# Performance work log

Hardware: AMD Instinct MI355X
Metric: run time of the kernel (lower is better)

The kernel has to match this reference:

```python
import jax, jax.numpy as jnp
import numpy as np

EPS = 1e-5


def _rln(x, w, b, m1w, m1b, m2w, m2b):
    # Revised LayerNorm (DehazeFormer): per-sample stats over (C,H,W)
    mean = jnp.mean(x, axis=(1, 2, 3), keepdims=True)            # [b,1,1,1]
    std = jnp.sqrt(jnp.mean((x - mean) ** 2, axis=(1, 2, 3), keepdims=True) + EPS)
    normed = (x - mean) / std * w + b                            # [b,C,H,W]
    rescale = std * m1w + m1b                                    # 1x1 conv from 1 channel
    rebias = mean * m2w + m2b
    return normed, rescale, rebias


def _pconv(x, W, b):
    # 1x1 conv as channel contraction: W [out,in], x [b,in,h,w]
    return jnp.einsum('oi,bihw->bohw', W, x) + b[None, :, None, None]


def setup_inputs() -> dict:
    key = jax.random.key(0)
    ks = jax.random.split(key, 24)
    B, C, H, W = 8, 96, 128, 128
    p = lambda k, shp, s=0.02: (jax.random.normal(k, shp, dtype=jnp.float32) * s)
    inp = {
        'x_u': jax.random.normal(ks[0], (B, C, H, W), dtype=jnp.float32),
        'x_d': jax.random.normal(ks[1], (B, C, H, W), dtype=jnp.float32),
        # RLN (u)
        'nw_u': jnp.ones((1, C, 1, 1), jnp.float32),
        'nb_u': jnp.zeros((1, C, 1, 1), jnp.float32),
        'm1w_u': p(ks[2], (1, C, 1, 1)), 'm1b_u': p(ks[3], (1, C, 1, 1)),
        'm2w_u': p(ks[4], (1, C, 1, 1)), 'm2b_u': p(ks[5], (1, C, 1, 1)),
        # RLN (d)
        'nw_d': jnp.ones((1, C, 1, 1), jnp.float32),
        'nb_d': jnp.zeros((1, C, 1, 1), jnp.float32),
        'm1w_d': p(ks[6], (1, C, 1, 1)), 'm1b_d': p(ks[7], (1, C, 1, 1)),
        'm2w_d': p(ks[8], (1, C, 1, 1)), 'm2b_d': p(ks[9], (1, C, 1, 1)),
        # 1x1 qkv convs
        'Wqkv_u': p(ks[10], (2 * C, C)), 'bqkv_u': jnp.zeros((2 * C,), jnp.float32),
        'Wqkv_d': p(ks[11], (2 * C, C)), 'bqkv_d': jnp.zeros((2 * C,), jnp.float32),
        # learned scalar scales
        'scale_h': jnp.ones((1,), jnp.float32),
        'scale_w': jnp.ones((1,), jnp.float32),
        'scale_c': jnp.ones((1,), jnp.float32),
    }
    return inp


def reference(x_u, x_d,
              nw_u, nb_u, m1w_u, m1b_u, m2w_u, m2b_u,
              nw_d, nb_d, m1w_d, m1b_d, m2w_d, m2b_d,
              Wqkv_u, bqkv_u, Wqkv_d, bqkv_d,
              scale_h, scale_w, scale_c):
    x_d_norm, resc_d, bias_d = _rln(x_d, nw_d, nb_d, m1w_d, m1b_d, m2w_d, m2b_d)
    x_u_norm, resc_u, bias_u = _rln(x_u, nw_u, nb_u, m1w_u, m1b_u, m2w_u, m2b_u)

    q_u, v_u = jnp.split(_pconv(x_u_norm, Wqkv_u, bqkv_u), 2, axis=1)
    k_d, v_d = jnp.split(_pconv(x_d_norm, Wqkv_d, bqkv_d), 2, axis=1)

    q_h, q_w, q_c = jnp.split(q_u, 3, axis=1)
    k_h, k_w, k_c = jnp.split(k_d, 3, axis=1)
    vu_h, vu_w, vu_c = jnp.split(v_u, 3, axis=1)
    vd_h, vd_w, vd_c = jnp.split(v_d, 3, axis=1)

    # ---- height-axis attention: per (b,w), scores over h x h ----
    A_h = jax.nn.softmax(jnp.einsum('bciw,bcjw->bwij', q_h, k_h) * scale_h[0], axis=-1)
    d2u_h = jnp.einsum('bwij,bcjw->bciw', A_h, vd_h)            # attn @ v_d
    u2d_h = jnp.einsum('bwij,bciw->bcjw', A_h, vu_h)            # attn^T @ v_u

    # ---- width-axis attention: per (b,h), scores over w x w ----
    S_w = jnp.einsum('bchi,bchj->bhij', q_w, k_w) * scale_w[0]
    d2u_w = jnp.einsum('bhij,bchj->bchi', jax.nn.softmax(S_w, axis=-1), vd_w)
    # softmax(S_w^T, -1) @ v_u  ==  softmax over axis -2, contracted over i
    u2d_w = jnp.einsum('bhij,bchi->bchj', jax.nn.softmax(S_w, axis=-2), vu_w)

    # ---- channel-axis attention: per b, scores over c x c ----
    b, c, h, w = q_c.shape
    qc = q_c.reshape(b, c, h * w)
    kc = k_c.reshape(b, c, h * w)
    A_c = jax.nn.softmax(jnp.einsum('bcn,bdn->bcd', qc, kc) * scale_c[0], axis=-1)
    d2u_c = jnp.einsum('bcd,bdn->bcn', A_c, vd_c.reshape(b, c, h * w)).reshape(b, c, h, w)
    # NOTE: original code uses the same (non-transposed) softmax for u2d_c
    u2d_c = jnp.einsum('bcd,bdn->bcn', A_c, vu_c.reshape(b, c, h * w)).reshape(b, c, h, w)

    x_d2u = jnp.concatenate([d2u_h, d2u_w, d2u_c], axis=1)
    x_u2d = jnp.concatenate([u2d_h, u2d_w, u2d_c], axis=1)

    out_u = x_d2u * resc_u + bias_u + x_u
    out_d = x_u2d * resc_d + bias_d + x_d
    return out_u + out_d
```

## Files before the change

kernel.cpp:

```cpp
#include <hip/hip_runtime.h>
#include <math.h>

#define NB 8
#define NC 96
#define NH 128
#define NWID 128
#define NN (NH*NWID)
#define NCO 192
#define NM (NC*NN)

#define WS_SUMS   0
#define WS_SC     32
#define WS_AC     8224
#define WS_SU     16416
#define WS_TU     17184
#define WS_SD     17952
#define WS_TD     18720
#define WS_RU     19488
#define WS_RD     20256
#define WS_CADD   21024
#define WS_BPU    21792
#define WS_BPD    23328
#define WS_WB16   24864
#define WS_QKV16  327680
#define QKV16_D   25165824ull
#define WS_SLABS  25493504
#define SLAB_SZ   4194304ull
#define OFF_QH    (0*SLAB_SZ)
#define OFF_KH    (1*SLAB_SZ)
#define OFF_QW    (2*SLAB_SZ)
#define OFF_KW    (3*SLAB_SZ)
#define OFF_VHU   (4*SLAB_SZ)
#define OFF_VHD   (5*SLAB_SZ)
#define OFF_VWU   (6*SLAB_SZ)
#define OFF_VWD   (7*SLAB_SZ)
#define WS_OH     44892160

typedef __attribute__((ext_vector_type(8))) short bf16x8;
typedef __attribute__((ext_vector_type(4))) float f32x4;

static __device__ __forceinline__ float bf2f(ushort u){ return __uint_as_float(((uint)u) << 16); }
static __device__ __forceinline__ ushort f2bf(float f){
  uint b = __float_as_uint(f);
  return (ushort)((b + 0x7fffu + ((b >> 16) & 1u)) >> 16);
}
static __device__ __forceinline__ bf16x8 ldfrag(const ushort* p){
  union { uint4 u; bf16x8 b; } cv; cv.u = *(const uint4*)p; return cv.b;
}

__global__ __launch_bounds__(256) void reduce_stats(const float* __restrict__ xu,
                                                    const float* __restrict__ xd,
                                                    float* __restrict__ ws) {
  int blk = blockIdx.x;
  int tensor = blk >> 9;
  int b = (blk >> 6) & 7;
  int chunk = blk & 63;
  const float* x = tensor ? xd : xu;
  const float4* p = (const float4*)(x + (size_t)b*NM + (size_t)chunk*(NM/64));
  float s = 0.f, sq = 0.f;
  for (int r = 0; r < 24; r++) {
    float4 v = p[threadIdx.x + r*256];
    s  += v.x + v.y + v.z + v.w;
    sq += v.x*v.x + v.y*v.y + v.z*v.z + v.w*v.w;
  }
  for (int o = 32; o; o >>= 1) { s += __shfl_down(s, o); sq += __shfl_down(sq, o); }
  __shared__ float ls[8];
  int wv = threadIdx.x >> 6, ln = threadIdx.x & 63;
  if (ln == 0) { ls[wv*2] = s; ls[wv*2+1] = sq; }
  __syncthreads();
  if (threadIdx.x == 0) {
    s  = ls[0] + ls[2] + ls[4] + ls[6];
    sq = ls[1] + ls[3] + ls[5] + ls[7];
    atomicAdd(&ws[WS_SUMS + (tensor*8 + b)*2],     s);
    atomicAdd(&ws[WS_SUMS + (tensor*8 + b)*2 + 1], sq);
  }
}

__global__ void compute_params(float* __restrict__ ws,
    const float* __restrict__ nwu, const float* __restrict__ nbu,
    const float* __restrict__ m1wu, const float* __restrict__ m1bu,
    const float* __restrict__ m2wu, const float* __restrict__ m2bu,
    const float* __restrict__ nwd, const float* __restrict__ nbd,
    const float* __restrict__ m1wd, const float* __restrict__ m1bd,
    const float* __restrict__ m2wd, const float* __restrict__ m2bd,
    const float* __restrict__ Wqu, const float* __restrict__ bqu,
    const float* __restrict__ Wqd, const float* __restrict__ bqd) {
  __shared__ float meanL[16], stdL[16];
  __shared__ float tuL[768], tdL[768];
  int t = threadIdx.x;
  if (t < 16) {
    float s = ws[WS_SUMS + t*2], sq = ws[WS_SUMS + t*2 + 1];
    const float inv = 1.f / (float)NM;
    float mean = s * inv;
    float var  = sq * inv - mean*mean;
    meanL[t] = mean;
    stdL[t]  = sqrtf(var + 1e-5f);
  }
  __syncthreads();
  for (int idx = t; idx < 768; idx += 256) {
    int b = idx / 96, c = idx % 96;
    float mu = meanL[b],   su = stdL[b];
    float md = meanL[8+b], sd = stdL[8+b];
    float scu = nwu[c] / su;
    float scd = nwd[c] / sd;
    float tcu = nbu[c] - mu*scu;
    float tcd = nbd[c] - md*scd;
    tuL[idx] = tcu; tdL[idx] = tcd;
    ws[WS_SU+idx] = scu; ws[WS_TU+idx] = tcu;
    ws[WS_SD+idx] = scd; ws[WS_TD+idx] = tcd;
    ws[WS_RU+idx] = su*m1wu[c] + m1bu[c];
    ws[WS_RD+idx] = sd*m1wd[c] + m1bd[c];
    ws[WS_CADD+idx] = (mu*m2wu[c] + m2bu[c]) + (md*m2wd[c] + m2bd[c]);
  }
  __syncthreads();
  for (int idx = t; idx < 3072; idx += 256) {
    int tensor = idx / 1536;
    int r = idx % 1536;
    int b = r / 192, o = r % 192;
    const float* Wq = tensor ? Wqd : Wqu;
    const float* tt = tensor ? tdL : tuL;
    float acc = tensor ? bqd[o] : bqu[o];
    for (int i = 0; i < 96; i++) acc += Wq[o*96 + i] * tt[b*96 + i];
    ws[(tensor ? WS_BPD : WS_BPU) + r] = acc;
  }
}

__global__ __launch_bounds__(256) void compute_wprime(float* __restrict__ ws,
    const float* __restrict__ Wqu, const float* __restrict__ Wqd) {
  int idx = blockIdx.x*256 + threadIdx.x;
  if (idx >= 319488) return;
  int tensor = idx / 159744;
  int r = idx % 159744;
  int b  = r / 19968;
  int r2 = r % 19968;
  int o  = r2 / 104, i = r2 % 104;
  ushort* wb = (ushort*)(ws + WS_WB16);
  ushort v = 0;
  if (i < 96) {
    const float* Wq = tensor ? Wqd : Wqu;
    const float* s  = ws + (tensor ? WS_SD : WS_SU);
    v = f2bf(Wq[o*96 + i] * s[b*96 + i]);
  }
  wb[idx] = v;
}

__global__ __launch_bounds__(256) void qkv_gemm(float* __restrict__ ws,
    const float* __restrict__ xu, const float* __restrict__ xd) {
  __shared__ __align__(16) ushort QL[16640];
  ushort* Bl = QL;
  ushort* Ah = QL + 6656;
  int blk = blockIdx.x;
  int tensor = blk >> 11;
  int rem = blk & 2047;
  int b = rem >> 8;
  int r2 = rem & 255;
  int nt = r2 >> 1;
  int wh = r2 & 1;
  int n0 = nt*128 + wh*64;
  const float* x = (tensor ? xd : xu) + (size_t)b*NM;
  const ushort* wb = (const ushort*)(ws + WS_WB16) + (size_t)(tensor*8 + b)*19968;
  const float* bp = ws + (tensor ? WS_BPD : WS_BPU) + b*192;
  ushort* outq16 = (ushort*)(ws + WS_QKV16) + (tensor ? QKV16_D : 0) + (size_t)b*NCO*NN;
  ushort* slab = (ushort*)(ws + WS_SLABS);
  const int t = threadIdx.x;
  const int wv = t >> 6, lid = t & 63, l15 = lid & 15, l4 = lid >> 4;

  for (int it = 0; it < 3; it++) {
    int idx = t + it*256;
    int i2 = (idx & 7) | ((idx >> 7) << 3);
    int n4 = (idx >> 3) & 15;
    const float* r0 = x + (size_t)(2*i2)*NN + n0 + n4*4;
    float4 a0 = *(const float4*)r0;
    float4 a1 = *(const float4*)(r0 + NN);
    uint p0 = (uint)f2bf(a0.x) | ((uint)f2bf(a1.x) << 16);
    uint p1 = (uint)f2bf(a0.y) | ((uint)f2bf(a1.y) << 16);
    uint p2 = (uint)f2bf(a0.z) | ((uint)f2bf(a1.z) << 16);
    uint p3 = (uint)f2bf(a0.w) | ((uint)f2bf(a1.w) << 16);
    ushort* base = &Bl[(size_t)(n4*4)*104 + 2*i2];
    *(uint*)(base)           = p0;
    *(uint*)(base + 104)     = p1;
    *(uint*)(base + 208)     = p2;
    *(uint*)(base + 312)     = p3;
  }
  for (int it = 0; it < 5; it++) {
    int idx = t + it*256;
    if (idx < 1248) ((uint4*)Ah)[idx] = ((const uint4*)wb)[idx];
  }
  __syncthreads();

  bf16x8 bfr[3];
  #pragma unroll
  for (int s = 0; s < 3; s++)
    bfr[s] = ldfrag(&Bl[(wv*16 + l15)*104 + s*32 + l4*8]);

  f32x4 z4 = {0.f,0.f,0.f,0.f};
  f32x4 acc[12];
  #pragma unroll
  for (int mt = 0; mt < 12; mt++) acc[mt] = z4;
  #pragma unroll
  for (int s = 0; s < 3; s++) {
    #pragma unroll
    for (int mt = 0; mt < 6; mt++) {
      bf16x8 a = ldfrag(&Ah[(mt*16 + l15)*104 + s*32 + l4*8]);
      acc[mt] = __builtin_amdgcn_mfma_f32_16x16x32_bf16(a, bfr[s], acc[mt], 0, 0, 0);
    }
  }
  __syncthreads();
  for (int it = 0; it < 5; it++) {
    int idx = t + it*256;
    if (idx < 1248) ((uint4*)Ah)[idx] = ((const uint4*)wb)[1248 + idx];
  }
  __syncthreads();
  #pragma unroll
  for (int s = 0; s < 3; s++) {
    #pragma unroll
    for (int mt = 0; mt < 6; mt++) {
      bf16x8 a = ldfrag(&Ah[(mt*16 + l15)*104 + s*32 + l4*8]);
      acc[6+mt] = __builtin_amdgcn_mfma_f32_16x16x32_bf16(a, bfr[s], acc[6+mt], 0, 0, 0);
    }
  }
  __syncthreads();
  ushort* Cl = QL;
  #pragma unroll
  for (int mt = 0; mt < 12; mt++) {
    #pragma unroll
    for (int r = 0; r < 4; r++) {
      int o = mt*16 + l4*4 + r;
      Cl[o*72 + wv*16 + l15] = f2bf(acc[mt][r] + bp[o]);
    }
  }
  __syncthreads();
  for (int it = 0; it < 3; it++) {
    int idx = t + it*256;
    int lr = idx >> 3, ch = idx & 7;
    int o = (lr < 64) ? (64 + lr) : (96 + lr);
    *(uint4*)(outq16 + (size_t)o*NN + n0 + ch*8) = *(const uint4*)&Cl[o*72 + ch*8];
  }
  if (t < 128) {
    int axis = t >> 6, w = t & 63;
    ushort* dstq = slab + (tensor ? (axis ? OFF_KW : OFF_KH) : (axis ? OFF_QW : OFF_QH));
    size_t o = axis ? ((size_t)(b*128 + nt)*128 + wh*64 + w)*32
                    : ((size_t)(b*128 + wh*64 + w)*128 + nt)*32;
    uint uu[16];
    #pragma unroll
    for (int k = 0; k < 16; k++) {
      ushort a0 = Cl[(axis*32 + 2*k)*72 + w];
      ushort a1 = Cl[(axis*32 + 2*k + 1)*72 + w];
      uu[k] = (uint)a0 | ((uint)a1 << 16);
    }
    *(uint4*)(dstq + o)      = make_uint4(uu[0],uu[1],uu[2],uu[3]);
    *(uint4*)(dstq + o + 8)  = make_uint4(uu[4],uu[5],uu[6],uu[7]);
    *(uint4*)(dstq + o + 16) = make_uint4(uu[8],uu[9],uu[10],uu[11]);
    *(uint4*)(dstq + o + 24) = make_uint4(uu[12],uu[13],uu[14],uu[15]);
  }
  {
    ushort* dstv = slab + (tensor ? OFF_VWD : OFF_VWU);
    int c = t >> 3, ch = t & 7;
    *(uint4*)(dstv + ((size_t)(b*128 + nt)*32 + c)*128 + wh*64 + ch*8) =
        *(const uint4*)&Cl[(128 + c)*72 + ch*8];
  }
}

__global__ __launch_bounds__(256) void qkv_prep(float* __restrict__ ws) {
  __shared__ __align__(16) ushort Br[16*1320];
  int bid = blockIdx.x;
  int tensor = bid >> 8;
  int r = bid & 255;
  int cb = r >> 7, b = (r >> 4) & 7, hb = (r >> 2) & 3, wb = r & 3;
  const ushort* qkv16 = (const ushort*)(ws + WS_QKV16);
  const ushort* src = qkv16 + (tensor ? QKV16_D : 0)
                    + (size_t)b*NCO*NN + (size_t)(96 + cb*16)*NN;
  ushort* dst = (ushort*)(ws + WS_SLABS) + (tensor ? OFF_VHD : OFF_VHU);
  int t = threadIdx.x;
  for (int k = 0; k < 8; k++) {
    int idx = t + k*256;
    int c = idx >> 7, h = (idx >> 2) & 31, w8 = idx & 3;
    uint4 v = *(const uint4*)(src + (size_t)c*NN + (size_t)(hb*32 + h)*NWID + wb*32 + w8*8);
    *(uint4*)&Br[c*1320 + h*40 + w8*8] = v;
  }
  __syncthreads();
  for (int k = 0; k < 2; k++) {
    int idx = t + k*256;
    int w = idx >> 4, c = idx & 15;
    uint uu[16];
    #pragma unroll
    for (int hh = 0; hh < 16; hh++) {
      ushort a0 = Br[c*1320 + (2*hh)*40 + w];
      ushort a1 = Br[c*1320 + (2*hh+1)*40 + w];
      uu[hh] = (uint)a0 | ((uint)a1 << 16);
    }
    size_t o = ((size_t)(b*128 + wb*32 + w)*32 + cb*16 + c)*128 + hb*32;
    *(uint4*)(dst + o)      = make_uint4(uu[0],uu[1],uu[2],uu[3]);
    *(uint4*)(dst + o + 8)  = make_uint4(uu[4],uu[5],uu[6],uu[7]);
    *(uint4*)(dst + o + 16) = make_uint4(uu[8],uu[9],uu[10],uu[11]);
    *(uint4*)(dst + o + 24) = make_uint4(uu[12],uu[13],uu[14],uu[15]);
  }
}

template<int AXIS>
__global__ __launch_bounds__(256) void attn_mfma(float* __restrict__ ws,
    const float* __restrict__ xu, const float* __restrict__ xd,
    float* __restrict__ out, const float* __restrict__ scale_p) {
  __shared__ __align__(16) ushort Qs[128*40];
  __shared__ __align__(16) ushort Ks[128*40];
  __shared__ __align__(16) ushort Vds[32*136];
  __shared__ __align__(16) ushort Vus[32*136];
  __shared__ __align__(16) ushort Pl[128*136];
  __shared__ float m1s[128], l1s[128];
  const int b = blockIdx.x >> 7, p2 = blockIdx.x & 127;
  const int t = threadIdx.x;
  const int wv = t >> 6, lid = t & 63, l15 = lid & 15, l4 = lid >> 4;
  const ushort* slab = (const ushort*)(ws + WS_SLABS);
  const ushort* qsrc  = slab + (AXIS ? OFF_QW : OFF_QH) + (size_t)(b*128 + p2)*4096;
  const ushort* ksrc  = slab + (AXIS ? OFF_KW : OFF_KH) + (size_t)(b*128 + p2)*4096;
  const ushort* vdsrc = slab + (AXIS ? OFF_VWD : OFF_VHD) + (size_t)(b*128 + p2)*4096;
  const ushort* vusrc = slab + (AXIS ? OFF_VWU : OFF_VHU) + (size_t)(b*128 + p2)*4096;
  for (int i = t; i < 2048; i += 256) {
    if (i < 512) {
      int row = i >> 2, q = i & 3;
      *(uint4*)&Qs[row*40 + q*8] = *(const uint4*)(qsrc + row*32 + q*8);
    } else if (i < 1024) {
      int j = i - 512, row = j >> 2, q = j & 3;
      *(uint4*)&Ks[row*40 + q*8] = *(const uint4*)(ksrc + row*32 + q*8);
    } else if (i < 1536) {
      int j = i - 1024, row = j >> 4, ch = j & 15;
      *(uint4*)&Vds[row*136 + ch*8] = *(const uint4*)(vdsrc + row*128 + ch*8);
    } else {
      int j = i - 1536, row = j >> 4, ch = j & 15;
      *(uint4*)&Vus[row*136 + ch*8] = *(const uint4*)(vusrc + row*128 + ch*8);
    }
  }
  const float sc = scale_p[0];
  const int cbas = AXIS ? 32 : 0;
  float ruv0 = ws[WS_RU + b*96 + cbas + l15];
  float ruv1 = ws[WS_RU + b*96 + cbas + 16 + l15];
  float rdv0 = ws[WS_RD + b*96 + cbas + l15];
  float rdv1 = ws[WS_RD + b*96 + cbas + 16 + l15];
  __syncthreads();

  f32x4 z4 = {0.f,0.f,0.f,0.f};
  f32x4 s1[2][8];
  {
    bf16x8 bfr[8];
    #pragma unroll
    for (int tj = 0; tj < 8; tj++) bfr[tj] = ldfrag(&Ks[(tj*16 + l15)*40 + l4*8]);
    #pragma unroll
    for (int ti = 0; ti < 2; ti++) {
      bf16x8 a = ldfrag(&Qs[((2*wv+ti)*16 + l15)*40 + l4*8]);
      #pragma unroll
      for (int tj = 0; tj < 8; tj++)
        s1[ti][tj] = __builtin_amdgcn_mfma_f32_16x16x32_bf16(a, bfr[tj], z4, 0, 0, 0);
    }
  }
  #pragma unroll
  for (int ti = 0; ti < 2; ti++) {
    #pragma unroll
    for (int r = 0; r < 4; r++) {
      float mx = -3.0e38f;
      #pragma unroll
      for (int tj = 0; tj < 8; tj++) { float v = s1[ti][tj][r]*sc; s1[ti][tj][r] = v; mx = fmaxf(mx, v); }
      mx = fmaxf(mx, __shfl_xor(mx, 1)); mx = fmaxf(mx, __shfl_xor(mx, 2));
      mx = fmaxf(mx, __shfl_xor(mx, 4)); mx = fmaxf(mx, __shfl_xor(mx, 8));
      float sm = 0.f;
      #pragma unroll
      for (int tj = 0; tj < 8; tj++) { float e = __expf(s1[ti][tj][r] - mx); s1[ti][tj][r] = e; sm += e; }
      sm += __shfl_xor(sm, 1); sm += __shfl_xor(sm, 2); sm += __shfl_xor(sm, 4); sm += __shfl_xor(sm, 8);
      int row = 32*wv + ti*16 + l4*4 + r;
      if (l15 == 0) { m1s[row] = mx; l1s[row] = sm; }
      float inv = __fdividef(1.f, sm);
      #pragma unroll
      for (int tj = 0; tj < 8; tj++) Pl[row*136 + tj*16 + l15] = f2bf(s1[ti][tj][r]*inv);
    }
  }
  __syncthreads();
  f32x4 o1[2][2] = {{z4,z4},{z4,z4}};
  #pragma unroll
  for (int ks = 0; ks < 4; ks++) {
    bf16x8 bv0 = ldfrag(&Vds[l15*136 + ks*32 + l4*8]);
    bf16x8 bv1 = ldfrag(&Vds[(16 + l15)*136 + ks*32 + l4*8]);
    #pragma unroll
    for (int mt = 0; mt < 2; mt++) {
      bf16x8 a = ldfrag(&Pl[((2*wv+mt)*16 + l15)*136 + ks*32 + l4*8]);
      o1[mt][0] = __builtin_amdgcn_mfma_f32_16x16x32_bf16(a, bv0, o1[mt][0], 0, 0, 0);
      o1[mt][1] = __builtin_amdgcn_mfma_f32_16x16x32_bf16(a, bv1, o1[mt][1], 0, 0, 0);
    }
  }
  {
    bf16x8 bq[8];
    #pragma unroll
    for (int it = 0; it < 8; it++) bq[it] = ldfrag(&Qs[(it*16 + l15)*40 + l4*8]);
    #pragma unroll
    for (int tjt = 0; tjt < 2; tjt++) {
      bf16x8 a = ldfrag(&Ks[((2*wv+tjt)*16 + l15)*40 + l4*8]);
      #pragma unroll
      for (int it = 0; it < 8; it++)
        s1[tjt][it] = __builtin_amdgcn_mfma_f32_16x16x32_bf16(a, bq[it], z4, 0, 0, 0);
    }
  }
  if (AXIS == 1) {
    #pragma unroll
    for (int tjt = 0; tjt < 2; tjt++) {
      #pragma unroll
      for (int r = 0; r < 4; r++) {
        float mx = -3.0e38f;
        #pragma unroll
        for (int it = 0; it < 8; it++) { float v = s1[tjt][it][r]*sc; s1[tjt][it][r] = v; mx = fmaxf(mx, v); }
        mx = fmaxf(mx, __shfl_xor(mx, 1)); mx = fmaxf(mx, __shfl_xor(mx, 2));
        mx = fmaxf(mx, __shfl_xor(mx, 4)); mx = fmaxf(mx, __shfl_xor(mx, 8));
        float sm = 0.f;
        #pragma unroll
        for (int it = 0; it < 8; it++) { float e = __expf(s1[tjt][it][r] - mx); s1[tjt][it][r] = e; sm += e; }
        sm += __shfl_xor(sm, 1); sm += __shfl_xor(sm, 2); sm += __shfl_xor(sm, 4); sm += __shfl_xor(sm, 8);
        float inv = __fdividef(1.f, sm);
        #pragma unroll
        for (int it = 0; it < 8; it++) s1[tjt][it][r] *= inv;
      }
    }
  } else {
    float mi[8], li[8];
    #pragma unroll
    for (int it = 0; it < 8; it++) {
      mi[it] = m1s[it*16 + l15];
      li[it] = __fdividef(1.f, l1s[it*16 + l15]);
    }
    #pragma unroll
    for (int tjt = 0; tjt < 2; tjt++)
      #pragma unroll
      for (int it = 0; it < 8; it++)
        #pragma unroll
        for (int r = 0; r < 4; r++)
          s1[tjt][it][r] = __expf(s1[tjt][it][r]*sc - mi[it]) * li[it];
  }
  __syncthreads();
  #pragma unroll
  for (int tjt = 0; tjt < 2; tjt++)
    #pragma unroll
    for (int r = 0; r < 4; r++) {
      int row = 32*wv + tjt*16 + l4*4 + r;
      #pragma unroll
      for (int it = 0; it < 8; it++) Pl[row*136 + it*16 + l15] = f2bf(s1[tjt][it][r]);
    }
  __syncthreads();
  f32x4 o2[2][2] = {{z4,z4},{z4,z4}};
  #pragma unroll
  for (int ks = 0; ks < 4; ks++) {
    bf16x8 bv0 = ldfrag(&Vus[l15*136 + ks*32 + l4*8]);
    bf16x8 bv1 = ldfrag(&Vus[(16 + l15)*136 + ks*32 + l4*8]);
    #pragma unroll
    for (int mt = 0; mt < 2; mt++) {
      bf16x8 a = ldfrag(&Pl[((2*wv+mt)*16 + l15)*136 + ks*32 + l4*8]);
      o2[mt][0] = __builtin_amdgcn_mfma_f32_16x16x32_bf16(a, bv0, o2[mt][0], 0, 0, 0);
      o2[mt][1] = __builtin_amdgcn_mfma_f32_16x16x32_bf16(a, bv1, o2[mt][1], 0, 0, 0);
    }
  }
  __syncthreads();
  float* St = (float*)Pl;
  #pragma unroll
  for (int mt = 0; mt < 2; mt++)
    #pragma unroll
    for (int nt = 0; nt < 2; nt++) {
      float ru = nt ? ruv1 : ruv0;
      float rd = nt ? rdv1 : rdv0;
      float4 vv;
      vv.x = o1[mt][nt][0]*ru + o2[mt][nt][0]*rd;
      vv.y = o1[mt][nt][1]*ru + o2[mt][nt][1]*rd;
      vv.z = o1[mt][nt][2]*ru + o2[mt][nt][2]*rd;
      vv.w = o1[mt][nt][3]*ru + o2[mt][nt][3]*rd;
      *(float4*)&St[(nt*16 + l15)*132 + (2*wv+mt)*16 + l4*4] = vv;
    }
  __syncthreads();
  if (AXIS == 1) {
    for (int k = 0; k < 4; k++) {
      int idx = t + k*256;
      int c = idx >> 5, p4 = idx & 31;
      float4 v = *(const float4*)&St[c*132 + p4*4];
      float ca = ws[WS_CADD + b*96 + 32 + c];
      size_t off = ((size_t)(b*NC + 32 + c)*NH + p2)*NWID + p4*4;
      float4 a = *(const float4*)(xu + off);
      float4 dd = *(const float4*)(xd + off);
      v.x += ca + a.x + dd.x; v.y += ca + a.y + dd.y;
      v.z += ca + a.z + dd.z; v.w += ca + a.w + dd.w;
      *(float4*)(out + off) = v;
    }
  } else {
    ushort* oh16 = (ushort*)(ws + WS_OH);
    for (int k = 0; k < 2; k++) {
      int idx = t + k*256;
      int c = idx >> 4, p8 = idx & 15;
      const float* src = &St[c*132 + p8*8];
      uint4 pk;
      pk.x = (uint)f2bf(src[0]) | ((uint)f2bf(src[1]) << 16);
      pk.y = (uint)f2bf(src[2]) | ((uint)f2bf(src[3]) << 16);
      pk.z = (uint)f2bf(src[4]) | ((uint)f2bf(src[5]) << 16);
      pk.w = (uint)f2bf(src[6]) | ((uint)f2bf(src[7]) << 16);
      *(uint4*)(oh16 + ((size_t)(b*128 + p2)*32 + c)*128 + p8*8) = pk;
    }
  }
}

__global__ __launch_bounds__(256) void merge_h(float* __restrict__ ws,
    const float* __restrict__ xu, const float* __restrict__ xd,
    float* __restrict__ out) {
  __shared__ float T[32][33];
  int bid = blockIdx.x;
  int b = bid >> 9, c = (bid >> 4) & 31, ht = (bid >> 2) & 3, wt = bid & 3;
  int t = threadIdx.x;
  const ushort* oh16 = (const ushort*)(ws + WS_OH);
  {
    int w = t >> 3, hq = t & 7;
    uint2 v = *(const uint2*)(oh16 + ((size_t)(b*128 + wt*32 + w)*32 + c)*128 + ht*32 + hq*4);
    T[w][hq*4+0] = bf2f((ushort)(v.x & 0xffff));
    T[w][hq*4+1] = bf2f((ushort)(v.x >> 16));
    T[w][hq*4+2] = bf2f((ushort)(v.y & 0xffff));
    T[w][hq*4+3] = bf2f((ushort)(v.y >> 16));
  }
  __syncthreads();
  {
    int h = t >> 3, w4 = t & 7;
    float ca = ws[WS_CADD + b*96 + c];
    size_t off = ((size_t)(b*NC + c)*NH + ht*32 + h)*NWID + wt*32 + w4*4;
    float4 a = *(const float4*)(xu + off);
    float4 d = *(const float4*)(xd + off);
    float4 v;
    v.x = T[w4*4+0][h] + ca + a.x + d.x;
    v.y = T[w4*4+1][h] + ca + a.y + d.y;
    v.z = T[w4*4+2][h] + ca + a.z + d.z;
    v.w = T[w4*4+3][h] + ca + a.w + d.w;
    *(float4*)(out + off) = v;
  }
}

__global__ __launch_bounds__(256) void attn_c1(float* __restrict__ ws) {
  __shared__ float qs[32][260], ks[32][260];
  int b = blockIdx.x >> 6, chunk = blockIdx.x & 63;
  int n0 = chunk * 256;
  int t = threadIdx.x;
  const ushort* qkv16 = (const ushort*)(ws + WS_QKV16);
  const ushort* qp = qkv16 + ((size_t)b*NCO + 64)*NN + n0;
  const ushort* kp = qkv16 + QKV16_D + ((size_t)b*NCO + 64)*NN + n0;
  for (int r = 0; r < 4; r++) {
    int idx = t + r*256;
    int c = idx >> 5, n8 = idx & 31;
    uint4 v = *(const uint4*)(qp + (size_t)c*NN + n8*8);
    uint4 w = *(const uint4*)(kp + (size_t)c*NN + n8*8);
    float* q = &qs[c][n8*8];
    float* kk = &ks[c][n8*8];
    q[0] = bf2f((ushort)(v.x & 0xffff)); q[1] = bf2f((ushort)(v.x >> 16));
    q[2] = bf2f((ushort)(v.y & 0xffff)); q[3] = bf2f((ushort)(v.y >> 16));
    q[4] = bf2f((ushort)(v.z & 0xffff)); q[5] = bf2f((ushort)(v.z >> 16));
    q[6] = bf2f((ushort)(v.w & 0xffff)); q[7] = bf2f((ushort)(v.w >> 16));
    kk[0] = bf2f((ushort)(w.x & 0xffff)); kk[1] = bf2f((ushort)(w.x >> 16));
    kk[2] = bf2f((ushort)(w.y & 0xffff)); kk[3] = bf2f((ushort)(w.y >> 16));
    kk[4] = bf2f((ushort)(w.z & 0xffff)); kk[5] = bf2f((ushort)(w.z >> 16));
    kk[6] = bf2f((ushort)(w.w & 0xffff)); kk[7] = bf2f((ushort)(w.w >> 16));
  }
  __syncthreads();
  int d = t & 31, cbq = t >> 5;
  float a[4] = {0.f,0.f,0.f,0.f};
  for (int n4 = 0; n4 < 64; n4++) {
    float4 kv = *(const float4*)&ks[d][n4*4];
    #pragma unroll
    for (int r = 0; r < 4; r++) {
      float4 qv = *(const float4*)&qs[cbq + 8*r][n4*4];
      a[r] += qv.x*kv.x + qv.y*kv.y + qv.z*kv.z + qv.w*kv.w;
    }
  }
  #pragma unroll
  for (int r = 0; r < 4; r++)
    atomicAdd(&ws[WS_SC + b*1024 + (cbq + 8*r)*32 + d], a[r]);
}

__global__ void attn_c2(float* __restrict__ ws, const float* __restrict__ scale_p) {
  int b = blockIdx.x, c = threadIdx.x;
  if (c >= 32) return;
  float sc = scale_p[0];
  float row[32];
  float m = -3.0e38f;
  for (int d = 0; d < 32; d++) { row[d] = ws[WS_SC + b*1024 + c*32 + d] * sc; m = fmaxf(m, row[d]); }
  float s = 0.f;
  for (int d = 0; d < 32; d++) { row[d] = __expf(row[d] - m); s += row[d]; }
  float inv = 1.f / s;
  for (int d = 0; d < 32; d++) ws[WS_AC + b*1024 + c*32 + d] = row[d]*inv;
}

__global__ __launch_bounds__(256) void attn_c3(float* __restrict__ ws,
    const float* __restrict__ xu, const float* __restrict__ xd,
    float* __restrict__ out) {
  __shared__ float AsT[32][36];
  __shared__ float ruL[32], rdL[32], caL[32];
  int b = blockIdx.x >> 6, chunk = blockIdx.x & 63;
  int t = threadIdx.x;
  for (int r = 0; r < 4; r++) {
    int idx = t + r*256;
    int c = idx >> 5, d = idx & 31;
    AsT[d][c] = ws[WS_AC + b*1024 + idx];
  }
  if (t < 32) {
    ruL[t] = ws[WS_RU + b*96 + 64 + t];
    rdL[t] = ws[WS_RD + b*96 + 64 + t];
    caL[t] = ws[WS_CADD + b*96 + 64 + t];
  }
  __syncthreads();
  int n = chunk*256 + t;
  const ushort* qkv16 = (const ushort*)(ws + WS_QKV16);
  const ushort* vdp = qkv16 + QKV16_D + ((size_t)b*NCO + 160)*NN + n;
  const ushort* vup = qkv16 + ((size_t)b*NCO + 160)*NN + n;
  float acc1[32], acc2[32];
  #pragma unroll
  for (int c2 = 0; c2 < 32; c2++) { acc1[c2]=0.f; acc2[c2]=0.f; }
  for (int d = 0; d < 32; d++) {
    float vd = bf2f(vdp[(size_t)d*NN]);
    float vu = bf2f(vup[(size_t)d*NN]);
    #pragma unroll
    for (int c4 = 0; c4 < 8; c4++) {
      float4 av = *(const float4*)&AsT[d][c4*4];
      acc1[c4*4+0] += av.x*vd; acc2[c4*4+0] += av.x*vu;
      acc1[c4*4+1] += av.y*vd; acc2[c4*4+1] += av.y*vu;
      acc1[c4*4+2] += av.z*vd; acc2[c4*4+2] += av.z*vu;
      acc1[c4*4+3] += av.w*vd; acc2[c4*4+3] += av.w*vu;
    }
  }
  size_t base = ((size_t)(b*NC) + 64)*NN + n;
  #pragma unroll
  for (int c2 = 0; c2 < 32; c2++) {
    size_t off = base + (size_t)c2*NN;
    out[off] = acc1[c2]*ruL[c2] + acc2[c2]*rdL[c2] + caL[c2] + xu[off] + xd[off];
  }
}

extern "C" void kernel_launch(void* const* d_in, const int* in_sizes, int n_in,
                              void* d_out, int out_size, void* d_ws, size_t ws_size,
                              hipStream_t stream) {
  (void)in_sizes; (void)n_in; (void)out_size; (void)ws_size;
  const float* xu   = (const float*)d_in[0];
  const float* xd   = (const float*)d_in[1];
  const float* nwu  = (const float*)d_in[2];
  const float* nbu  = (const float*)d_in[3];
  const float* m1wu = (const float*)d_in[4];
  const float* m1bu = (const float*)d_in[5];
  const float* m2wu = (const float*)d_in[6];
  const float* m2bu = (const float*)d_in[7];
  const float* nwd  = (const float*)d_in[8];
  const float* nbd  = (const float*)d_in[9];
  const float* m1wd = (const float*)d_in[10];
  const float* m1bd = (const float*)d_in[11];
  const float* m2wd = (const float*)d_in[12];
  const float* m2bd = (const float*)d_in[13];
  const float* Wqu  = (const float*)d_in[14];
  const float* bqu  = (const float*)d_in[15];
  const float* Wqd  = (const float*)d_in[16];
  const float* bqd  = (const float*)d_in[17];
  const float* sch  = (const float*)d_in[18];
  const float* scw  = (const float*)d_in[19];
  const float* scc  = (const float*)d_in[20];
  float* ws  = (float*)d_ws;
  float* out = (float*)d_out;

  hipMemsetAsync(d_ws, 0, 8224*sizeof(float), stream);
  reduce_stats<<<1024, 256, 0, stream>>>(xu, xd, ws);
  compute_params<<<1, 256, 0, stream>>>(ws, nwu, nbu, m1wu, m1bu, m2wu, m2bu,
                                        nwd, nbd, m1wd, m1bd, m2wd, m2bd,
                                        Wqu, bqu, Wqd, bqd);
  compute_wprime<<<1248, 256, 0, stream>>>(ws, Wqu, Wqd);
  qkv_gemm<<<4096, 256, 0, stream>>>(ws, xu, xd);
  qkv_prep<<<512, 256, 0, stream>>>(ws);
  attn_mfma<0><<<1024, 256, 0, stream>>>(ws, xu, xd, out, sch);
  attn_mfma<1><<<1024, 256, 0, stream>>>(ws, xu, xd, out, scw);
  merge_h<<<4096, 256, 0, stream>>>(ws, xu, xd, out);
  attn_c1<<<512, 256, 0, stream>>>(ws);
  attn_c2<<<8, 64, 0, stream>>>(ws, scc);
  attn_c3<<<512, 256, 0, stream>>>(ws, xu, xd, out);
}
```

Measured before the change: 248.6 us.

## Fold weight-scaling into QKV GEMM and merge attention launches into one grid

Removes the separate compute_wprime kernel: each qkv_gemm block now reads fp32 weights, multiplies them by the per-sample RLN scale, and converts to bf16 while staging into shared memory. It also merges the height-axis, width-axis and channel-score attention kernels into a single launch, choosing the role from blockIdx and sharing one union shared-memory buffer. This cuts launch count and tail gaps, and lets channel-score blocks overlap with axis-attention blocks. In exchange, every GEMM block redoes the weight scaling and reads more global data, and the union shared buffer may limit occupancy for the smaller channel blocks.

```diff
diff --git a/kernel.cpp b/kernel.cpp
--- a/kernel.cpp
+++ b/kernel.cpp
@@ -21,7 +21,6 @@
 #define WS_CADD   21024
 #define WS_BPU    21792
 #define WS_BPD    23328
-#define WS_WB16   24864
 #define WS_QKV16  327680
 #define QKV16_D   25165824ull
 #define WS_SLABS  25493504
@@ -125,27 +124,9 @@
   }
 }
 
-__global__ __launch_bounds__(256) void compute_wprime(float* __restrict__ ws,
+__global__ __launch_bounds__(256) void qkv_gemm(float* __restrict__ ws,
+    const float* __restrict__ xu, const float* __restrict__ xd,
     const float* __restrict__ Wqu, const float* __restrict__ Wqd) {
-  int idx = blockIdx.x*256 + threadIdx.x;
-  if (idx >= 319488) return;
-  int tensor = idx / 159744;
-  int r = idx % 159744;
-  int b  = r / 19968;
-  int r2 = r % 19968;
-  int o  = r2 / 104, i = r2 % 104;
-  ushort* wb = (ushort*)(ws + WS_WB16);
-  ushort v = 0;
-  if (i < 96) {
-    const float* Wq = tensor ? Wqd : Wqu;
-    const float* s  = ws + (tensor ? WS_SD : WS_SU);
-    v = f2bf(Wq[o*96 + i] * s[b*96 + i]);
-  }
-  wb[idx] = v;
-}
-
-__global__ __launch_bounds__(256) void qkv_gemm(float* __restrict__ ws,
-    const float* __restrict__ xu, const float* __restrict__ xd) {
   __shared__ __align__(16) ushort QL[16640];
   ushort* Bl = QL;
   ushort* Ah = QL + 6656;
@@ -158,7 +139,8 @@
   int wh = r2 & 1;
   int n0 = nt*128 + wh*64;
   const float* x = (tensor ? xd : xu) + (size_t)b*NM;
-  const ushort* wb = (const ushort*)(ws + WS_WB16) + (size_t)(tensor*8 + b)*19968;
+  const float* Wq = tensor ? Wqd : Wqu;
+  const float* sca = ws + (tensor ? WS_SD : WS_SU) + b*96;
   const float* bp = ws + (tensor ? WS_BPD : WS_BPU) + b*192;
   ushort* outq16 = (ushort*)(ws + WS_QKV16) + (tensor ? QKV16_D : 0) + (size_t)b*NCO*NN;
   ushort* slab = (ushort*)(ws + WS_SLABS);
@@ -182,9 +164,12 @@
     *(uint*)(base + 208)     = p2;
     *(uint*)(base + 312)     = p3;
   }
-  for (int it = 0; it < 5; it++) {
+  for (int it = 0; it < 18; it++) {
     int idx = t + it*256;
-    if (idx < 1248) ((uint4*)Ah)[idx] = ((const uint4*)wb)[idx];
+    int o = idx / 48, ip = idx % 48;
+    float2 wv2 = *(const float2*)(Wq + (size_t)o*96 + 2*ip);
+    float2 sv  = *(const float2*)(sca + 2*ip);
+    *(uint*)&Ah[o*104 + 2*ip] = (uint)f2bf(wv2.x*sv.x) | ((uint)f2bf(wv2.y*sv.y) << 16);
   }
   __syncthreads();
 
@@ -206,9 +191,12 @@
     }
   }
   __syncthreads();
-  for (int it = 0; it < 5; it++) {
+  for (int it = 0; it < 18; it++) {
     int idx = t + it*256;
-    if (idx < 1248) ((uint4*)Ah)[idx] = ((const uint4*)wb)[1248 + idx];
+    int o = idx / 48, ip = idx % 48;
+    float2 wv2 = *(const float2*)(Wq + (size_t)(96 + o)*96 + 2*ip);
+    float2 sv  = *(const float2*)(sca + 2*ip);
+    *(uint*)&Ah[o*104 + 2*ip] = (uint)f2bf(wv2.x*sv.x) | ((uint)f2bf(wv2.y*sv.y) << 16);
   }
   __syncthreads();
   #pragma unroll
@@ -297,18 +285,63 @@
   }
 }
 
-template<int AXIS>
-__global__ __launch_bounds__(256) void attn_mfma(float* __restrict__ ws,
+__global__ __launch_bounds__(256) void attn_both(float* __restrict__ ws,
     const float* __restrict__ xu, const float* __restrict__ xd,
-    float* __restrict__ out, const float* __restrict__ scale_p) {
-  __shared__ __align__(16) ushort Qs[128*40];
-  __shared__ __align__(16) ushort Ks[128*40];
-  __shared__ __align__(16) ushort Vds[32*136];
-  __shared__ __align__(16) ushort Vus[32*136];
-  __shared__ __align__(16) ushort Pl[128*136];
+    float* __restrict__ out, const float* __restrict__ sch, const float* __restrict__ scw) {
+  __shared__ __align__(16) ushort SMEM[36352];
   __shared__ float m1s[128], l1s[128];
-  const int b = blockIdx.x >> 7, p2 = blockIdx.x & 127;
   const int t = threadIdx.x;
+
+  if (blockIdx.x >= 2048) {
+    float* qs = (float*)SMEM;
+    float* ks = qs + 8320;
+    int bid = blockIdx.x - 2048;
+    int b = bid >> 6, chunk = bid & 63;
+    int n0 = chunk * 256;
+    const ushort* qkv16 = (const ushort*)(ws + WS_QKV16);
+    const ushort* qp = qkv16 + ((size_t)b*NCO + 64)*NN + n0;
+    const ushort* kp = qkv16 + QKV16_D + ((size_t)b*NCO + 64)*NN + n0;
+    for (int r = 0; r < 4; r++) {
+      int idx = t + r*256;
+      int c = idx >> 5, n8 = idx & 31;
+      uint4 v = *(const uint4*)(qp + (size_t)c*NN + n8*8);
+      uint4 w = *(const uint4*)(kp + (size_t)c*NN + n8*8);
+      float* q  = &qs[c*260 + n8*8];
+      float* kk = &ks[c*260 + n8*8];
+      q[0] = bf2f((ushort)(v.x & 0xffff)); q[1] = bf2f((ushort)(v.x >> 16));
+      q[2] = bf2f((ushort)(v.y & 0xffff)); q[3] = bf2f((ushort)(v.y >> 16));
+      q[4] = bf2f((ushort)(v.z & 0xffff)); q[5] = bf2f((ushort)(v.z >> 16));
+      q[6] = bf2f((ushort)(v.w & 0xffff)); q[7] = bf2f((ushort)(v.w >> 16));
+      kk[0] = bf2f((ushort)(w.x & 0xffff)); kk[1] = bf2f((ushort)(w.x >> 16));
+      kk[2] = bf2f((ushort)(w.y & 0xffff)); kk[3] = bf2f((ushort)(w.y >> 16));
+      kk[4] = bf2f((ushort)(w.z & 0xffff)); kk[5] = bf2f((ushort)(w.z >> 16));
+      kk[6] = bf2f((ushort)(w.w & 0xffff)); kk[7] = bf2f((ushort)(w.w >> 16));
+    }
+    __syncthreads();
+    int d = t & 31, cbq = t >> 5;
+    float a[4] = {0.f,0.f,0.f,0.f};
+    for (int n4 = 0; n4 < 64; n4++) {
+      float4 kv = *(const float4*)&ks[d*260 + n4*4];
+      #pragma unroll
+      for (int r = 0; r < 4; r++) {
+        float4 qv = *(const float4*)&qs[(cbq + 8*r)*260 + n4*4];
+        a[r] += qv.x*kv.x + qv.y*kv.y + qv.z*kv.z + qv.w*kv.w;
+      }
+    }
+    #pragma unroll
+    for (int r = 0; r < 4; r++)
+      atomicAdd(&ws[WS_SC + b*1024 + (cbq + 8*r)*32 + d], a[r]);
+    return;
+  }
+
+  ushort* Qs  = SMEM;
+  ushort* Ks  = SMEM + 5120;
+  ushort* Vds = SMEM + 10240;
+  ushort* Vus = SMEM + 14592;
+  ushort* Pl  = SMEM + 18944;
+  const int AXIS = blockIdx.x >> 10;
+  const int rem = blockIdx.x & 1023;
+  const int b = rem >> 7, p2 = rem & 127;
   const int wv = t >> 6, lid = t & 63, l15 = lid & 15, l4 = lid >> 4;
   const ushort* slab = (const ushort*)(ws + WS_SLABS);
   const ushort* qsrc  = slab + (AXIS ? OFF_QW : OFF_QH) + (size_t)(b*128 + p2)*4096;
@@ -330,7 +363,7 @@
       *(uint4*)&Vus[row*136 + ch*8] = *(const uint4*)(vusrc + row*128 + ch*8);
     }
   }
-  const float sc = scale_p[0];
+  const float sc = (AXIS ? scw : sch)[0];
   const int cbas = AXIS ? 32 : 0;
   float ruv0 = ws[WS_RU + b*96 + cbas + l15];
   float ruv1 = ws[WS_RU + b*96 + cbas + 16 + l15];
@@ -528,46 +561,6 @@
     v.w = T[w4*4+3][h] + ca + a.w + d.w;
     *(float4*)(out + off) = v;
   }
-}
-
-__global__ __launch_bounds__(256) void attn_c1(float* __restrict__ ws) {
-  __shared__ float qs[32][260], ks[32][260];
-  int b = blockIdx.x >> 6, chunk = blockIdx.x & 63;
-  int n0 = chunk * 256;
-  int t = threadIdx.x;
-  const ushort* qkv16 = (const ushort*)(ws + WS_QKV16);
-  const ushort* qp = qkv16 + ((size_t)b*NCO + 64)*NN + n0;
-  const ushort* kp = qkv16 + QKV16_D + ((size_t)b*NCO + 64)*NN + n0;
-  for (int r = 0; r < 4; r++) {
-    int idx = t + r*256;
-    int c = idx >> 5, n8 = idx & 31;
-    uint4 v = *(const uint4*)(qp + (size_t)c*NN + n8*8);
-    uint4 w = *(const uint4*)(kp + (size_t)c*NN + n8*8);
-    float* q = &qs[c][n8*8];
-    float* kk = &ks[c][n8*8];
-    q[0] = bf2f((ushort)(v.x & 0xffff)); q[1] = bf2f((ushort)(v.x >> 16));
-    q[2] = bf2f((ushort)(v.y & 0xffff)); q[3] = bf2f((ushort)(v.y >> 16));
-    q[4] = bf2f((ushort)(v.z & 0xffff)); q[5] = bf2f((ushort)(v.z >> 16));
-    q[6] = bf2f((ushort)(v.w & 0xffff)); q[7] = bf2f((ushort)(v.w >> 16));
-    kk[0] = bf2f((ushort)(w.x & 0xffff)); kk[1] = bf2f((ushort)(w.x >> 16));
-    kk[2] = bf2f((ushort)(w.y & 0xffff)); kk[3] = bf2f((ushort)(w.y >> 16));
-    kk[4] = bf2f((ushort)(w.z & 0xffff)); kk[5] = bf2f((ushort)(w.z >> 16));
-    kk[6] = bf2f((ushort)(w.w & 0xffff)); kk[7] = bf2f((ushort)(w.w >> 16));
-  }
-  __syncthreads();
-  int d = t & 31, cbq = t >> 5;
-  float a[4] = {0.f,0.f,0.f,0.f};
-  for (int n4 = 0; n4 < 64; n4++) {
-    float4 kv = *(const float4*)&ks[d][n4*4];
-    #pragma unroll
-    for (int r = 0; r < 4; r++) {
-      float4 qv = *(const float4*)&qs[cbq + 8*r][n4*4];
-      a[r] += qv.x*kv.x + qv.y*kv.y + qv.z*kv.z + qv.w*kv.w;
-    }
-  }
-  #pragma unroll
-  for (int r = 0; r < 4; r++)
-    atomicAdd(&ws[WS_SC + b*1024 + (cbq + 8*r)*32 + d], a[r]);
 }
 
 __global__ void attn_c2(float* __restrict__ ws, const float* __restrict__ scale_p) {
@@ -661,13 +654,10 @@
   compute_params<<<1, 256, 0, stream>>>(ws, nwu, nbu, m1wu, m1bu, m2wu, m2bu,
                                         nwd, nbd, m1wd, m1bd, m2wd, m2bd,
                                         Wqu, bqu, Wqd, bqd);
-  compute_wprime<<<1248, 256, 0, stream>>>(ws, Wqu, Wqd);
-  qkv_gemm<<<4096, 256, 0, stream>>>(ws, xu, xd);
+  qkv_gemm<<<4096, 256, 0, stream>>>(ws, xu, xd, Wqu, Wqd);
   qkv_prep<<<512, 256, 0, stream>>>(ws);
-  attn_mfma<0><<<1024, 256, 0, stream>>>(ws, xu, xd, out, sch);
-  attn_mfma<1><<<1024, 256, 0, stream>>>(ws, xu, xd, out, scw);
+  attn_both<<<2560, 256, 0, stream>>>(ws, xu, xd, out, sch, scw);
   merge_h<<<4096, 256, 0, stream>>>(ws, xu, xd, out);
-  attn_c1<<<512, 256, 0, stream>>>(ws);
   attn_c2<<<8, 64, 0, stream>>>(ws, scc);
   attn_c3<<<512, 256, 0, stream>>>(ws, xu, xd, out);
 }
```

New measurement: 258.9 us. 1.04x slower.
